# Kernel tuning notes

Hardware: AMD Instinct MI355X
Metric: run time of the kernel (lower is better)

## Reference

```python
import jax, jax.numpy as jnp
import numpy as np

SAMPLE_RATE = 22050
N_FILTER_BANKS = 64
HOP_LENGTH = 512
BATCH = 4
N_FRAMES = 500
N_SAMPLES = N_FRAMES * HOP_LENGTH


def _frame_mean_weights(n_frames, n_samples):
    """Per-frame weights w s.t. mean over time of linear(align_corners=True)
    upsampling of a length-n_frames signal equals w @ signal (exact same math,
    since the interpolation is linear in the frame values)."""
    pos = jnp.linspace(0.0, n_frames - 1.0, n_samples)
    lo = jnp.clip(jnp.floor(pos).astype(jnp.int32), 0, n_frames - 2)
    frac = pos - lo
    w = jnp.zeros(n_frames, dtype=jnp.float32)
    w = w.at[lo].add(1.0 - frac).at[lo + 1].add(frac)
    return w / n_samples


def setup_inputs() -> dict:
    key = jax.random.key(0)
    k1, k2 = jax.random.split(key)
    filter_magnitudes = jax.random.uniform(k1, (BATCH, N_FRAMES, N_FILTER_BANKS), dtype=jnp.float32)
    noise = jax.random.normal(k2, (BATCH, N_SAMPLES), dtype=jnp.float32)
    return {"filter_magnitudes": filter_magnitudes, "noise": noise}


def reference(filter_magnitudes, noise):
    B, n_frames, n_banks = filter_magnitudes.shape
    n_samples = noise.shape[1]

    noise_fft = jnp.fft.rfft(noise, axis=1)                      # (B, n_freq) complex
    freqs = jnp.fft.rfftfreq(n_samples, 1.0 / SAMPLE_RATE)       # (n_freq,)
    filter_freqs = jnp.logspace(np.log10(20.0), np.log10(SAMPLE_RATE / 2.0), n_banks).astype(jnp.float32)

    # mean over time of the linearly-upsampled magnitudes (exact, no big buffer)
    mean_w = _frame_mean_weights(n_frames, n_samples)            # (n_frames,)
    mean_mag = jnp.einsum('bfk,f->bk', filter_magnitudes, mean_w)  # (B, n_banks)

    # vectorized log-distance filterbank weights: (n_freq, n_banks)
    D = jnp.log(freqs + 1e-7)[:, None] - jnp.log(filter_freqs + 1e-7)[None, :]
    W = jnp.exp(-(D ** 2) / 0.5)
    W = W / (W.sum(axis=1, keepdims=True) + 1e-7)

    filter_response = mean_mag @ W.T                              # (B, n_freq)
    filtered_fft = noise_fft * filter_response
    return jnp.fft.irfft(filtered_fft, n=n_samples, axis=1)      # (B, n_samples)
```

## Files before the change

kernel.cpp:

```cpp
#include <hip/hip_runtime.h>
#include <math.h>

#define NS 256000
#define N1 512
#define N2 500
#define PI_F 3.14159265358979323846f

typedef float2 cplx;

__device__ __forceinline__ cplx cadd(cplx a, cplx b){ return make_float2(a.x+b.x, a.y+b.y); }
__device__ __forceinline__ cplx csub(cplx a, cplx b){ return make_float2(a.x-b.x, a.y-b.y); }
__device__ __forceinline__ cplx cmul(cplx a, cplx b){ return make_float2(a.x*b.x-a.y*b.y, a.x*b.y+a.y*b.x); }
__device__ __forceinline__ cplx cmulc(cplx a, cplx b){ return make_float2(a.x*b.x+a.y*b.y, a.y*b.x-a.x*b.y); }
__device__ __forceinline__ cplx crotf(cplx v, float ang){
    float sn = __sinf(ang), cs = __cosf(ang);
    return make_float2(v.x*cs - v.y*sn, v.x*sn + v.y*cs);
}
__device__ __forceinline__ int PX(int e){ return e + (e>>4); }
__device__ __forceinline__ int rev8_3(int k){ return ((k&7)<<6) | (k&0x38) | (k>>6); }

#define U1PAD 545
#define U2PAD 537
#define WFENCE() asm volatile("s_waitcnt lgkmcnt(0)" ::: "memory")

template<bool INV>
__device__ __forceinline__ void dft4(const cplx* a, cplx* b){
    cplx t0=cadd(a[0],a[2]), t1=csub(a[0],a[2]), t2=cadd(a[1],a[3]), t3=csub(a[1],a[3]);
    b[0]=cadd(t0,t2); b[2]=csub(t0,t2);
    if(!INV){ b[1]=make_float2(t1.x+t3.y, t1.y-t3.x); b[3]=make_float2(t1.x-t3.y, t1.y+t3.x); }
    else    { b[1]=make_float2(t1.x-t3.y, t1.y+t3.x); b[3]=make_float2(t1.x+t3.y, t1.y-t3.x); }
}

template<bool INV>
__device__ __forceinline__ void dft8(const cplx* a, cplx* b){
    cplx ev[4]={a[0],a[2],a[4],a[6]}, od[4]={a[1],a[3],a[5],a[7]};
    cplx C[4], D[4];
    dft4<INV>(ev, C); dft4<INV>(od, D);
    const float s = 0.70710678118654752f;
    const float sg = INV ? 1.f : -1.f;
    cplx d1 = cmul(D[1], make_float2( s, sg*s));
    cplx d2 = cmul(D[2], make_float2(0.f, sg ));
    cplx d3 = cmul(D[3], make_float2(-s, sg*s));
    b[0]=cadd(C[0],D[0]); b[4]=csub(C[0],D[0]);
    b[1]=cadd(C[1],d1);   b[5]=csub(C[1],d1);
    b[2]=cadd(C[2],d2);   b[6]=csub(C[2],d2);
    b[3]=cadd(C[3],d3);   b[7]=csub(C[3],d3);
}

template<bool INV>
__device__ __forceinline__ void dft5(const cplx* a, cplx* b){
    const float c1=0.30901699437494742f, s1=0.95105651629515357f;
    const float c2=-0.80901699437494745f, s2=0.58778525229247312f;
    const float sg = INV ? 1.f : -1.f;
    cplx W[5];
    W[0]=make_float2(1.f,0.f);
    W[1]=make_float2(c1, sg*s1); W[2]=make_float2(c2, sg*s2);
    W[3]=make_float2(c2,-sg*s2); W[4]=make_float2(c1,-sg*s1);
#pragma unroll
    for(int u=0;u<5;++u){
        cplx acc = a[0];
        int idx = 0;
#pragma unroll
        for(int r=1;r<5;++r){
            idx += u; if(idx >= 5) idx -= 5;
            acc = cadd(acc, cmul(a[r], W[idx]));
        }
        b[u] = acc;
    }
}

template<int R, int L, int TMUL, bool INV, int NN>
__device__ __forceinline__ void wstage(cplx* Uw, const cplx* tab, int lane){
    constexpr int m = L / R;
    constexpr int nb = NN / R;
    constexpr int NIT = (nb + 63) / 64;
    cplx a[NIT][R];
    cplx wt[NIT][R];
    int  bs[NIT];
#pragma unroll
    for(int it=0; it<NIT; ++it){
        int beta = lane + it*64;
        int blk = beta / m;
        int j = beta - blk*m;
        bs[it] = blk*L + j;
        if(beta < nb){
#pragma unroll
            for(int t=0;t<R;++t) a[it][t] = Uw[PX(bs[it] + m*t)];
#pragma unroll
            for(int t=1;t<R;++t) wt[it][t] = tab[TMUL*j*t];
        }
    }
#pragma unroll
    for(int it=0; it<NIT; ++it){
        int beta = lane + it*64;
        if(beta < nb){
            if(INV){
#pragma unroll
                for(int t=1;t<R;++t) a[it][t] = cmulc(a[it][t], wt[it][t]);
            }
            cplx bb[R];
            if constexpr (R==4) dft4<INV>(a[it], bb);
            else if constexpr (R==5) dft5<INV>(a[it], bb);
            else dft8<INV>(a[it], bb);
            if(!INV){
#pragma unroll
                for(int t=1;t<R;++t) bb[t] = cmul(bb[t], wt[it][t]);
            }
#pragma unroll
            for(int t=0;t<R;++t) Uw[PX(bs[it] + m*t)] = bb[t];
        }
    }
}

template<int NTAB>
__device__ __forceinline__ void build_tab(cplx* tab, int tid){
    const float step = -2.f*PI_F/(float)NTAB;
    for(int i = tid; i < NTAB; i += 128){
        float a = step*(float)i;
        tab[i] = make_float2(__cosf(a), __sinf(a));
    }
}

__device__ __forceinline__ int p2k2(int p){
    int t1 = p/100; int r = p - 100*t1;
    int t2 = r/20;  r -= 20*t2;
    int t3 = r>>2;  int t4 = r & 3;
    return t1 + 5*t2 + 25*t3 + 125*t4;
}
__device__ __forceinline__ int k22p(int k){
    int t1 = k % 5; int k5 = k/5;
    int t2 = k5 % 5; int k25 = k5/5;
    int t3 = k25 % 5; int t4 = k25/5;
    return 100*t1 + 20*t2 + 4*t3 + t4;
}
__device__ __forceinline__ int colord(int q){
    int j = q>>1, w = q&1;
    if(j == 0) return w ? 256 : 0;
    return w ? 512 - j : j;
}
__device__ __forceinline__ int xcd_chunk(int bid, int n){
    int q = n>>3, r = n&7;
    int x = bid&7, idx = bid>>3;
    return (x < r ? x*(q+1) : r*(q+1) + (x-r)*q) + idx;
}

__device__ __forceinline__ void hpair(cplx Z1, cplx Z2, float ha, float hb,
                                      cplx* zk, cplx* znk){
    float xr = 0.5f*(Z1.x + Z2.x), xi = 0.5f*(Z1.y - Z2.y);
    float yr = 0.5f*(Z1.y + Z2.y), yi = -0.5f*(Z1.x - Z2.x);
    *zk  = make_float2(ha*xr - hb*yi, ha*xi + hb*yr);
    *znk = make_float2(ha*xr + hb*yi, hb*yr - ha*xi);
}

__global__ void __launch_bounds__(128) kFused1(const float* __restrict__ fm,
                                               const float* __restrict__ noise,
                                               float* __restrict__ mmL,
                                               cplx* __restrict__ Y){
    __shared__ float Aarr[500];
    __shared__ float wfr[500];
    __shared__ float part[128];
    __shared__ cplx tab[512];
    __shared__ cplx U[2][U1PAD];
    const int bid = blockIdx.x, tid = threadIdx.x;
    if(bid < 4){
        const int b = bid;
        for(int f = tid; f < 500; f += 128){
            long long i0 = ((long long)f*255999LL + 498LL)/499LL;
            long long i1 = ((long long)(f+1)*255999LL + 498LL)/499LL;
            long long cnt = i1 - i0;
            long long sumi = (i0 + i1 - 1)*cnt/2;
            long long num = 499LL*sumi - cnt*(long long)f*255999LL;
            Aarr[f] = (float)((double)num / 255999.0);
        }
        __syncthreads();
        for(int f = tid; f < 500; f += 128){
            long long i0 = ((long long)f*255999LL + 498LL)/499LL;
            long long i1 = ((long long)(f+1)*255999LL + 498LL)/499LL;
            double w;
            if(f < 499) w = (double)(i1 - i0) - (double)Aarr[f] + (f > 0 ? (double)Aarr[f-1] : 0.0);
            else        w = (double)Aarr[498] + 1.0;
            wfr[f] = (float)(w / (double)NS);
        }
        __syncthreads();
        const int k = tid & 63, seg = tid >> 6;
        float acc = 0.f;
        for(int f = seg*250; f < seg*250 + 250; ++f)
            acc += wfr[f] * fm[(b*500 + f)*64 + k];
        part[seg*64 + k] = acc;
        __syncthreads();
        if(tid < 64) mmL[b*64 + tid] = part[tid] + part[64 + tid];
        return;
    }
    if(bid == 4){
        if(tid < 64){
            double a = log10(20.0), b2 = log10(11025.0);
            double e = a + (b2 - a)*(double)tid/63.0;
            float ff = (float)pow(10.0, e);
            mmL[256 + tid] = logf(ff + 1e-7f);
        }
        return;
    }
    const int g = bid - 5;
    const int s = g / 250;
    const int n2base = (g - s*250) * 2;
    const int lane = tid & 63, w = tid >> 6;
    build_tab<512>(tab, tid);
    const float* xa = noise + (size_t)(2*s)*NS + n2base;
    const float* xb = noise + (size_t)(2*s+1)*NS + n2base;
#pragma unroll
    for(int k=0;k<8;++k){
        int i = tid + 128*k;
        int n1 = i >> 1, ws = i & 1;
        U[ws][PX(n1)] = make_float2(xa[n1*500 + ws], xb[n1*500 + ws]);
    }
    __syncthreads();
    cplx* Uw = U[w];
    wstage<8,512, 1,false,512>(Uw, tab, lane); WFENCE();
    wstage<8, 64, 8,false,512>(Uw, tab, lane); WFENCE();
    wstage<8,  8,64,false,512>(Uw, tab, lane); WFENCE();
    const int n2 = n2base + w;
    cplx* yp = Y + ((size_t)s*500 + n2)*512;
    const float tw = -2.f*PI_F/(float)NS;
#pragma unroll
    for(int t=0;t<8;++t){
        int q = lane + 64*t;
        int c = colord(q);
        cplx v = Uw[PX(rev8_3(c))];
        v = crotf(v, tw*(float)(n2*c));
        yp[q] = v;
    }
}

__global__ void __launch_bounds__(128) kFused2(cplx* __restrict__ Y,
                                               const float* __restrict__ mmL){
    __shared__ cplx tab[500];
    __shared__ cplx U[2][U2PAD];
    __shared__ float Hr[4][500];
    __shared__ float mmS[2][64];
    __shared__ float lgf[64];
    const int tid = threadIdx.x, lane = tid & 63, w = tid >> 6;
    const int L = xcd_chunk(blockIdx.x, 512);
    const int s = L >> 8, blk = L & 255;
    build_tab<500>(tab, tid);
    if(tid < 128) mmS[tid>>6][tid&63] = mmL[2*s*64 + tid];
    if(tid < 64)  lgf[tid] = mmL[256 + tid];
    cplx* yb = Y + (size_t)s*500*512 + 2*blk;
    cplx rg[8];
#pragma unroll
    for(int k=0;k<8;++k){
        int i = tid + 128*k;
        rg[k] = (i < 1000) ? yb[(i>>1)*512 + (i&1)] : make_float2(0.f, 0.f);
    }
    __syncthreads();
    const int nrows = (blk == 0) ? 2 : 1;
    const float invN = 1.f/(float)NS;
    for(int idx = tid; idx < nrows*500; idx += 128){
        int r = (idx >= 500) ? 1 : 0;
        int p = idx - 500*r;
        int k1 = (blk == 0) ? (r ? 256 : 0) : blk;
        int k2 = p2k2(p);
        int kf = k1 + 512*k2;
        int kk = min(kf, NS - kf);
        float lf = logf((float)kk*(22050.f/(float)NS) + 1e-7f);
        float wsum = 0.f, a0 = 0.f, a1 = 0.f;
#pragma unroll
        for(int jb=0;jb<64;++jb){
            float d = lf - lgf[jb];
            float e = __expf(-2.f*d*d);
            wsum += e; a0 += e*mmS[0][jb]; a1 += e*mmS[1][jb];
        }
        float inv = invN/(wsum + 1e-7f);
        Hr[2*r  ][p] = a0*inv;
        Hr[2*r+1][p] = a1*inv;
    }
#pragma unroll
    for(int k=0;k<8;++k){
        int i = tid + 128*k;
        if(i < 1000) U[i&1][PX(i>>1)] = rg[k];
    }
    __syncthreads();
    cplx* Uw = U[w];
    wstage<5,500,  1,false,500>(Uw, tab, lane); WFENCE();
    wstage<5,100,  5,false,500>(Uw, tab, lane); WFENCE();
    wstage<5, 20, 25,false,500>(Uw, tab, lane); WFENCE();
    wstage<4,  4,125,false,500>(Uw, tab, lane); WFENCE();
    __syncthreads();
    if(blk == 0){
        if(w == 0){
#pragma unroll
            for(int t=0;t<8;++t){
                int p = lane + 64*t;
                if(p < 500){
                    int k2 = p2k2(p);
                    int pp = k22p((500 - k2) % 500);
                    if(p <= pp){
                        cplx Z1 = U[0][PX(p)], Z2 = U[0][PX(pp)];
                        cplx zk, znk;
                        hpair(Z1, Z2, Hr[0][p], Hr[1][p], &zk, &znk);
                        U[0][PX(p)]  = zk;
                        U[0][PX(pp)] = znk;
                    }
                }
            }
        } else {
#pragma unroll
            for(int t=0;t<4;++t){
                int p = lane + 64*t;
                if(p < 250){
                    cplx Z1 = U[1][PX(p)], Z2 = U[1][PX(499-p)];
                    cplx zk, znk;
                    hpair(Z1, Z2, Hr[2][p], Hr[3][p], &zk, &znk);
                    U[1][PX(p)]     = zk;
                    U[1][PX(499-p)] = znk;
                }
            }
        }
    } else {
#pragma unroll
        for(int t=0;t<4;++t){
            int pl = lane + 64*t;
            if(pl < 250){
                int p = w*250 + pl;
                cplx Z1 = U[0][PX(p)], Z2 = U[1][PX(499-p)];
                cplx zk, znk;
                hpair(Z1, Z2, Hr[0][p], Hr[1][p], &zk, &znk);
                U[0][PX(p)]     = zk;
                U[1][PX(499-p)] = znk;
            }
        }
    }
    __syncthreads();
    wstage<4,  4,125,true,500>(Uw, tab, lane); WFENCE();
    wstage<5, 20, 25,true,500>(Uw, tab, lane); WFENCE();
    wstage<5,100,  5,true,500>(Uw, tab, lane); WFENCE();
    wstage<5,500,  1,true,500>(Uw, tab, lane); WFENCE();
    __syncthreads();
    const float tw = 2.f*PI_F/(float)NS;
#pragma unroll
    for(int k=0;k<8;++k){
        int i = tid + 128*k;
        if(i < 1000){
            int n2 = i >> 1, ws = i & 1;
            int c = colord(2*blk + ws);
            cplx v = U[ws][PX(n2)];
            v = crotf(v, tw*(float)(n2*c));
            yb[n2*512 + ws] = v;
        }
    }
}

__global__ void __launch_bounds__(128) kFused3(const cplx* __restrict__ Y,
                                               float* __restrict__ out){
    __shared__ cplx tab[512];
    __shared__ cplx U[2][U1PAD];
    const int tid = threadIdx.x, lane = tid & 63, w = tid >> 6;
    const int L = xcd_chunk(blockIdx.x, 500);
    const int s = L / 250;
    const int n2base = (L - s*250) * 2;
    build_tab<512>(tab, tid);
    const cplx* yp = Y + ((size_t)s*500 + n2base)*512;
#pragma unroll
    for(int k=0;k<8;++k){
        int i = tid + 128*k;
        int ws = i >> 9, q = i & 511;
        cplx v = yp[(size_t)ws*512 + q];
        U[ws][PX(rev8_3(colord(q)))] = v;
    }
    __syncthreads();
    cplx* Uw = U[w];
    wstage<8,  8,64,true,512>(Uw, tab, lane); WFENCE();
    wstage<8, 64, 8,true,512>(Uw, tab, lane); WFENCE();
    wstage<8,512, 1,true,512>(Uw, tab, lane); WFENCE();
    __syncthreads();
    float* oa = out + (size_t)(2*s)*NS + n2base;
    float* ob = out + (size_t)(2*s+1)*NS + n2base;
#pragma unroll
    for(int k=0;k<8;++k){
        int i = tid + 128*k;
        int n1 = i >> 1, ws = i & 1;
        cplx v = U[ws][PX(n1)];
        oa[n1*500 + ws] = v.x;
        ob[n1*500 + ws] = v.y;
    }
}

extern "C" void kernel_launch(void* const* d_in, const int* in_sizes, int n_in,
                              void* d_out, int out_size, void* d_ws, size_t ws_size,
                              hipStream_t stream) {
    const float* fm = (const float*)d_in[0];
    const float* noise = (const float*)d_in[1];
    float* out = (float*)d_out;

    char* ws = (char*)d_ws;
    cplx*  Y   = (cplx*)ws;
    float* mmL = (float*)(ws + 4200000);

    kFused1<<<505, 128, 0, stream>>>(fm, noise, mmL, Y);
    kFused2<<<512, 128, 0, stream>>>(Y, mmL);
    kFused3<<<500, 128, 0, stream>>>(Y, out);
}
```

Before: 98.65 us.

## Widen FFT kernels to 256 threads and split column FFT stages across two waves

The row-FFT kernels (kFused1, kFused3) now process four columns per 256-thread block instead of two, which halves the number of blocks and shares the twiddle-table build across more work. kFused2 keeps two columns per block but assigns two waves to each column. It splits each radix stage's butterflies between them with a new wstage2 helper, so block-wide barriers are needed between stages. kFused2 also issues its global loads before building the twiddle table, to hide load latency. The aim is higher occupancy and latency hiding, at the cost of more synchronisation and fewer blocks in the first and last kernels.

```diff
diff --git a/kernel.cpp b/kernel.cpp
--- a/kernel.cpp
+++ b/kernel.cpp
@@ -22,6 +22,7 @@
 #define U1PAD 545
 #define U2PAD 537
 #define WFENCE() asm volatile("s_waitcnt lgkmcnt(0)" ::: "memory")
+#define LDS_BARRIER() do{ asm volatile("s_waitcnt lgkmcnt(0)" ::: "memory"); __builtin_amdgcn_s_barrier(); }while(0)
 
 template<bool INV>
 __device__ __forceinline__ void dft4(const cplx* a, cplx* b){
@@ -112,10 +113,44 @@
     }
 }
 
-template<int NTAB>
+template<int R, int L, int TMUL, bool INV>
+__device__ __forceinline__ void wstage2(cplx* Uc, const cplx* tab, int lane, int h){
+    constexpr int m = L / R;
+    constexpr int nb = 500 / R;
+    constexpr int HB = (nb + 1) / 2;
+    const int lim = h ? (nb - HB) : HB;
+    if(lane < lim){
+        int beta = h*HB + lane;
+        int blk = beta / m;
+        int j = beta - blk*m;
+        int base = blk*L + j;
+        cplx a[R];
+#pragma unroll
+        for(int t=0;t<R;++t) a[t] = Uc[PX(base + m*t)];
+        cplx wt[R];
+#pragma unroll
+        for(int t=1;t<R;++t) wt[t] = tab[TMUL*j*t];
+        if(INV){
+#pragma unroll
+            for(int t=1;t<R;++t) a[t] = cmulc(a[t], wt[t]);
+        }
+        cplx bb[R];
+        if constexpr (R==4) dft4<INV>(a,bb);
+        else if constexpr (R==5) dft5<INV>(a,bb);
+        else dft8<INV>(a,bb);
+        if(!INV){
+#pragma unroll
+            for(int t=1;t<R;++t) bb[t] = cmul(bb[t], wt[t]);
+        }
+#pragma unroll
+        for(int t=0;t<R;++t) Uc[PX(base + m*t)] = bb[t];
+    }
+}
+
+template<int NTAB, int NTHR>
 __device__ __forceinline__ void build_tab(cplx* tab, int tid){
     const float step = -2.f*PI_F/(float)NTAB;
-    for(int i = tid; i < NTAB; i += 128){
+    for(int i = tid; i < NTAB; i += NTHR){
         float a = step*(float)i;
         tab[i] = make_float2(__cosf(a), __sinf(a));
     }
@@ -152,19 +187,19 @@
     *znk = make_float2(ha*xr + hb*yi, hb*yr - ha*xi);
 }
 
-__global__ void __launch_bounds__(128) kFused1(const float* __restrict__ fm,
+__global__ void __launch_bounds__(256) kFused1(const float* __restrict__ fm,
                                                const float* __restrict__ noise,
                                                float* __restrict__ mmL,
                                                cplx* __restrict__ Y){
     __shared__ float Aarr[500];
     __shared__ float wfr[500];
-    __shared__ float part[128];
+    __shared__ float part[256];
     __shared__ cplx tab[512];
-    __shared__ cplx U[2][U1PAD];
+    __shared__ cplx U[4][U1PAD];
     const int bid = blockIdx.x, tid = threadIdx.x;
     if(bid < 4){
         const int b = bid;
-        for(int f = tid; f < 500; f += 128){
+        for(int f = tid; f < 500; f += 256){
             long long i0 = ((long long)f*255999LL + 498LL)/499LL;
             long long i1 = ((long long)(f+1)*255999LL + 498LL)/499LL;
             long long cnt = i1 - i0;
@@ -173,7 +208,7 @@
             Aarr[f] = (float)((double)num / 255999.0);
         }
         __syncthreads();
-        for(int f = tid; f < 500; f += 128){
+        for(int f = tid; f < 500; f += 256){
             long long i0 = ((long long)f*255999LL + 498LL)/499LL;
             long long i1 = ((long long)(f+1)*255999LL + 498LL)/499LL;
             double w;
@@ -184,11 +219,11 @@
         __syncthreads();
         const int k = tid & 63, seg = tid >> 6;
         float acc = 0.f;
-        for(int f = seg*250; f < seg*250 + 250; ++f)
+        for(int f = seg*125; f < seg*125 + 125; ++f)
             acc += wfr[f] * fm[(b*500 + f)*64 + k];
         part[seg*64 + k] = acc;
         __syncthreads();
-        if(tid < 64) mmL[b*64 + tid] = part[tid] + part[64 + tid];
+        if(tid < 64) mmL[b*64 + tid] = part[tid] + part[64+tid] + part[128+tid] + part[192+tid];
         return;
     }
     if(bid == 4){
@@ -200,17 +235,17 @@
         }
         return;
     }
-    const int g = bid - 5;
-    const int s = g / 250;
-    const int n2base = (g - s*250) * 2;
+    const int g = xcd_chunk(bid - 5, 250);
+    const int s = g / 125;
+    const int n2base = (g - s*125) * 4;
     const int lane = tid & 63, w = tid >> 6;
-    build_tab<512>(tab, tid);
+    build_tab<512,256>(tab, tid);
     const float* xa = noise + (size_t)(2*s)*NS + n2base;
     const float* xb = noise + (size_t)(2*s+1)*NS + n2base;
 #pragma unroll
     for(int k=0;k<8;++k){
-        int i = tid + 128*k;
-        int n1 = i >> 1, ws = i & 1;
+        int i = tid + 256*k;
+        int n1 = i >> 2, ws = i & 3;
         U[ws][PX(n1)] = make_float2(xa[n1*500 + ws], xb[n1*500 + ws]);
     }
     __syncthreads();
@@ -231,30 +266,30 @@
     }
 }
 
-__global__ void __launch_bounds__(128) kFused2(cplx* __restrict__ Y,
+__global__ void __launch_bounds__(256) kFused2(cplx* __restrict__ Y,
                                                const float* __restrict__ mmL){
     __shared__ cplx tab[500];
     __shared__ cplx U[2][U2PAD];
     __shared__ float Hr[4][500];
     __shared__ float mmS[2][64];
     __shared__ float lgf[64];
-    const int tid = threadIdx.x, lane = tid & 63, w = tid >> 6;
+    const int tid = threadIdx.x, lane = tid & 63, W = tid >> 6;
     const int L = xcd_chunk(blockIdx.x, 512);
     const int s = L >> 8, blk = L & 255;
-    build_tab<500>(tab, tid);
+    cplx* yb = Y + (size_t)s*500*512 + 2*blk;
+    cplx rg[4];
+#pragma unroll
+    for(int k=0;k<4;++k){
+        int i = tid + 256*k;
+        rg[k] = (i < 1000) ? yb[(i>>1)*512 + (i&1)] : make_float2(0.f, 0.f);
+    }
+    build_tab<500,256>(tab, tid);
     if(tid < 128) mmS[tid>>6][tid&63] = mmL[2*s*64 + tid];
     if(tid < 64)  lgf[tid] = mmL[256 + tid];
-    cplx* yb = Y + (size_t)s*500*512 + 2*blk;
-    cplx rg[8];
-#pragma unroll
-    for(int k=0;k<8;++k){
-        int i = tid + 128*k;
-        rg[k] = (i < 1000) ? yb[(i>>1)*512 + (i&1)] : make_float2(0.f, 0.f);
-    }
-    __syncthreads();
+    LDS_BARRIER();
     const int nrows = (blk == 0) ? 2 : 1;
     const float invN = 1.f/(float)NS;
-    for(int idx = tid; idx < nrows*500; idx += 128){
+    for(int idx = tid; idx < nrows*500; idx += 256){
         int r = (idx >= 500) ? 1 : 0;
         int p = idx - 500*r;
         int k1 = (blk == 0) ? (r ? 256 : 0) : blk;
@@ -270,27 +305,28 @@
             wsum += e; a0 += e*mmS[0][jb]; a1 += e*mmS[1][jb];
         }
         float inv = invN/(wsum + 1e-7f);
-        Hr[2*r  ][p] = a0*inv;
-        Hr[2*r+1][p] = a1*inv;
-    }
-#pragma unroll
-    for(int k=0;k<8;++k){
-        int i = tid + 128*k;
+        Hr[0][p] = (r==0) ? a0*inv : Hr[0][p];
+        if(r==0){ Hr[0][p] = a0*inv; Hr[1][p] = a1*inv; }
+        else    { Hr[2][p] = a0*inv; Hr[3][p] = a1*inv; }
+    }
+#pragma unroll
+    for(int k=0;k<4;++k){
+        int i = tid + 256*k;
         if(i < 1000) U[i&1][PX(i>>1)] = rg[k];
     }
     __syncthreads();
-    cplx* Uw = U[w];
-    wstage<5,500,  1,false,500>(Uw, tab, lane); WFENCE();
-    wstage<5,100,  5,false,500>(Uw, tab, lane); WFENCE();
-    wstage<5, 20, 25,false,500>(Uw, tab, lane); WFENCE();
-    wstage<4,  4,125,false,500>(Uw, tab, lane); WFENCE();
-    __syncthreads();
+    const int c = W >> 1, h = W & 1;
+    cplx* Uc = U[c];
+    wstage2<5,500,  1,false>(Uc, tab, lane, h); __syncthreads();
+    wstage2<5,100,  5,false>(Uc, tab, lane, h); __syncthreads();
+    wstage2<5, 20, 25,false>(Uc, tab, lane, h); __syncthreads();
+    wstage2<4,  4,125,false>(Uc, tab, lane, h); __syncthreads();
     if(blk == 0){
-        if(w == 0){
-#pragma unroll
-            for(int t=0;t<8;++t){
-                int p = lane + 64*t;
-                if(p < 500){
+        if(c == 0){
+#pragma unroll
+            for(int t=0;t<4;++t){
+                int p = h*250 + lane + 64*t;
+                if(lane + 64*t < 250){
                     int k2 = p2k2(p);
                     int pp = k22p((500 - k2) % 500);
                     if(p <= pp){
@@ -304,9 +340,10 @@
             }
         } else {
 #pragma unroll
-            for(int t=0;t<4;++t){
-                int p = lane + 64*t;
-                if(p < 250){
+            for(int t=0;t<2;++t){
+                int pl = lane + 64*t;
+                if(pl < 125){
+                    int p = h*125 + pl;
                     cplx Z1 = U[1][PX(p)], Z2 = U[1][PX(499-p)];
                     cplx zk, znk;
                     hpair(Z1, Z2, Hr[2][p], Hr[3][p], &zk, &znk);
@@ -317,10 +354,10 @@
         }
     } else {
 #pragma unroll
-        for(int t=0;t<4;++t){
+        for(int t=0;t<2;++t){
             int pl = lane + 64*t;
-            if(pl < 250){
-                int p = w*250 + pl;
+            if(pl < 125){
+                int p = W*125 + pl;
                 cplx Z1 = U[0][PX(p)], Z2 = U[1][PX(499-p)];
                 cplx zk, znk;
                 hpair(Z1, Z2, Hr[0][p], Hr[1][p], &zk, &znk);
@@ -330,38 +367,37 @@
         }
     }
     __syncthreads();
-    wstage<4,  4,125,true,500>(Uw, tab, lane); WFENCE();
-    wstage<5, 20, 25,true,500>(Uw, tab, lane); WFENCE();
-    wstage<5,100,  5,true,500>(Uw, tab, lane); WFENCE();
-    wstage<5,500,  1,true,500>(Uw, tab, lane); WFENCE();
-    __syncthreads();
+    wstage2<4,  4,125,true>(Uc, tab, lane, h); __syncthreads();
+    wstage2<5, 20, 25,true>(Uc, tab, lane, h); __syncthreads();
+    wstage2<5,100,  5,true>(Uc, tab, lane, h); __syncthreads();
+    wstage2<5,500,  1,true>(Uc, tab, lane, h); __syncthreads();
     const float tw = 2.f*PI_F/(float)NS;
 #pragma unroll
-    for(int k=0;k<8;++k){
-        int i = tid + 128*k;
+    for(int k=0;k<4;++k){
+        int i = tid + 256*k;
         if(i < 1000){
             int n2 = i >> 1, ws = i & 1;
-            int c = colord(2*blk + ws);
+            int cc = colord(2*blk + ws);
             cplx v = U[ws][PX(n2)];
-            v = crotf(v, tw*(float)(n2*c));
+            v = crotf(v, tw*(float)(n2*cc));
             yb[n2*512 + ws] = v;
         }
     }
 }
 
-__global__ void __launch_bounds__(128) kFused3(const cplx* __restrict__ Y,
+__global__ void __launch_bounds__(256) kFused3(const cplx* __restrict__ Y,
                                                float* __restrict__ out){
     __shared__ cplx tab[512];
-    __shared__ cplx U[2][U1PAD];
+    __shared__ cplx U[4][U1PAD];
     const int tid = threadIdx.x, lane = tid & 63, w = tid >> 6;
-    const int L = xcd_chunk(blockIdx.x, 500);
-    const int s = L / 250;
-    const int n2base = (L - s*250) * 2;
-    build_tab<512>(tab, tid);
+    const int g = xcd_chunk(blockIdx.x, 250);
+    const int s = g / 125;
+    const int n2base = (g - s*125) * 4;
+    build_tab<512,256>(tab, tid);
     const cplx* yp = Y + ((size_t)s*500 + n2base)*512;
 #pragma unroll
     for(int k=0;k<8;++k){
-        int i = tid + 128*k;
+        int i = tid + 256*k;
         int ws = i >> 9, q = i & 511;
         cplx v = yp[(size_t)ws*512 + q];
         U[ws][PX(rev8_3(colord(q)))] = v;
@@ -376,8 +412,8 @@
     float* ob = out + (size_t)(2*s+1)*NS + n2base;
 #pragma unroll
     for(int k=0;k<8;++k){
-        int i = tid + 128*k;
-        int n1 = i >> 1, ws = i & 1;
+        int i = tid + 256*k;
+        int n1 = i >> 2, ws = i & 3;
         cplx v = U[ws][PX(n1)];
         oa[n1*500 + ws] = v.x;
         ob[n1*500 + ws] = v.y;
@@ -395,7 +431,7 @@
     cplx*  Y   = (cplx*)ws;
     float* mmL = (float*)(ws + 4200000);
 
-    kFused1<<<505, 128, 0, stream>>>(fm, noise, mmL, Y);
-    kFused2<<<512, 128, 0, stream>>>(Y, mmL);
-    kFused3<<<500, 128, 0, stream>>>(Y, out);
-}
+    kFused1<<<255, 256, 0, stream>>>(fm, noise, mmL, Y);
+    kFused2<<<512, 256, 0, stream>>>(Y, mmL);
+    kFused3<<<250, 256, 0, stream>>>(Y, out);
+}
```

Measured after the change: 93.45 us. 1.06x faster.

## Double per-block FFT work to four columns with 256-thread blocks

Applied to the files above, without the earlier changes.

All three FFT kernels now run 256-thread blocks, each handling four columns or rows instead of two. That halves the grid sizes, gives 4-wide contiguous global accesses, and remaps kFused1 blocks through the XCD chunking. kFused2 loads its global data before building the twiddle table, uses a cheaper LDS barrier, and drops some trailing waitcnt fences. The intent is to cut per-block overhead (twiddle table builds, launch cost) and improve coalescing, at the cost of fewer blocks for the GPU's many CUs and higher LDS use per block.

```diff
diff --git a/kernel.cpp b/kernel.cpp
--- a/kernel.cpp
+++ b/kernel.cpp
@@ -22,6 +22,7 @@
 #define U1PAD 545
 #define U2PAD 537
 #define WFENCE() asm volatile("s_waitcnt lgkmcnt(0)" ::: "memory")
+#define LDS_BARRIER() do{ asm volatile("s_waitcnt lgkmcnt(0)" ::: "memory"); __builtin_amdgcn_s_barrier(); }while(0)
 
 template<bool INV>
 __device__ __forceinline__ void dft4(const cplx* a, cplx* b){
@@ -112,10 +113,10 @@
     }
 }
 
-template<int NTAB>
+template<int NTAB, int NTHR>
 __device__ __forceinline__ void build_tab(cplx* tab, int tid){
     const float step = -2.f*PI_F/(float)NTAB;
-    for(int i = tid; i < NTAB; i += 128){
+    for(int i = tid; i < NTAB; i += NTHR){
         float a = step*(float)i;
         tab[i] = make_float2(__cosf(a), __sinf(a));
     }
@@ -152,19 +153,19 @@
     *znk = make_float2(ha*xr + hb*yi, hb*yr - ha*xi);
 }
 
-__global__ void __launch_bounds__(128) kFused1(const float* __restrict__ fm,
+__global__ void __launch_bounds__(256) kFused1(const float* __restrict__ fm,
                                                const float* __restrict__ noise,
                                                float* __restrict__ mmL,
                                                cplx* __restrict__ Y){
     __shared__ float Aarr[500];
     __shared__ float wfr[500];
-    __shared__ float part[128];
+    __shared__ float part[256];
     __shared__ cplx tab[512];
-    __shared__ cplx U[2][U1PAD];
+    __shared__ cplx U[4][U1PAD];
     const int bid = blockIdx.x, tid = threadIdx.x;
     if(bid < 4){
         const int b = bid;
-        for(int f = tid; f < 500; f += 128){
+        for(int f = tid; f < 500; f += 256){
             long long i0 = ((long long)f*255999LL + 498LL)/499LL;
             long long i1 = ((long long)(f+1)*255999LL + 498LL)/499LL;
             long long cnt = i1 - i0;
@@ -173,7 +174,7 @@
             Aarr[f] = (float)((double)num / 255999.0);
         }
         __syncthreads();
-        for(int f = tid; f < 500; f += 128){
+        for(int f = tid; f < 500; f += 256){
             long long i0 = ((long long)f*255999LL + 498LL)/499LL;
             long long i1 = ((long long)(f+1)*255999LL + 498LL)/499LL;
             double w;
@@ -184,11 +185,11 @@
         __syncthreads();
         const int k = tid & 63, seg = tid >> 6;
         float acc = 0.f;
-        for(int f = seg*250; f < seg*250 + 250; ++f)
+        for(int f = seg*125; f < seg*125 + 125; ++f)
             acc += wfr[f] * fm[(b*500 + f)*64 + k];
         part[seg*64 + k] = acc;
         __syncthreads();
-        if(tid < 64) mmL[b*64 + tid] = part[tid] + part[64 + tid];
+        if(tid < 64) mmL[b*64 + tid] = part[tid] + part[64+tid] + part[128+tid] + part[192+tid];
         return;
     }
     if(bid == 4){
@@ -200,17 +201,17 @@
         }
         return;
     }
-    const int g = bid - 5;
-    const int s = g / 250;
-    const int n2base = (g - s*250) * 2;
+    const int g = xcd_chunk(bid - 5, 250);
+    const int s = g / 125;
+    const int n2base = (g - s*125) * 4;
     const int lane = tid & 63, w = tid >> 6;
-    build_tab<512>(tab, tid);
+    build_tab<512,256>(tab, tid);
     const float* xa = noise + (size_t)(2*s)*NS + n2base;
     const float* xb = noise + (size_t)(2*s+1)*NS + n2base;
 #pragma unroll
     for(int k=0;k<8;++k){
-        int i = tid + 128*k;
-        int n1 = i >> 1, ws = i & 1;
+        int i = tid + 256*k;
+        int n1 = i >> 2, ws = i & 3;
         U[ws][PX(n1)] = make_float2(xa[n1*500 + ws], xb[n1*500 + ws]);
     }
     __syncthreads();
@@ -219,7 +220,7 @@
     wstage<8, 64, 8,false,512>(Uw, tab, lane); WFENCE();
     wstage<8,  8,64,false,512>(Uw, tab, lane); WFENCE();
     const int n2 = n2base + w;
-    cplx* yp = Y + ((size_t)s*500 + n2)*512;
+    cplx* yp = Y + ((size_t)s*500 + n2)*N1;
     const float tw = -2.f*PI_F/(float)NS;
 #pragma unroll
     for(int t=0;t<8;++t){
@@ -231,33 +232,37 @@
     }
 }
 
-__global__ void __launch_bounds__(128) kFused2(cplx* __restrict__ Y,
+__global__ void __launch_bounds__(256) kFused2(cplx* __restrict__ Y,
                                                const float* __restrict__ mmL){
     __shared__ cplx tab[500];
-    __shared__ cplx U[2][U2PAD];
-    __shared__ float Hr[4][500];
+    __shared__ cplx U[4][U2PAD];
+    __shared__ float Hr[2][2][500];
+    __shared__ float HrX[2][500];
     __shared__ float mmS[2][64];
     __shared__ float lgf[64];
     const int tid = threadIdx.x, lane = tid & 63, w = tid >> 6;
-    const int L = xcd_chunk(blockIdx.x, 512);
-    const int s = L >> 8, blk = L & 255;
-    build_tab<500>(tab, tid);
-    if(tid < 128) mmS[tid>>6][tid&63] = mmL[2*s*64 + tid];
+    const int L = xcd_chunk(blockIdx.x, 256);
+    const int su = L >> 7;
+    const int j0 = 2*(L & 127);
+    const int s0 = 2*j0;
+    cplx* Ybase = Y + (size_t)su*500*512 + s0;
+    cplx rg[8];
+#pragma unroll
+    for(int k=0;k<8;++k){
+        int e = tid + 256*k;
+        rg[k] = (e < 2000) ? Ybase[(e>>2)*512 + (e&3)] : make_float2(0.f,0.f);
+    }
+    build_tab<500,256>(tab, tid);
+    if(tid < 128) mmS[tid>>6][tid&63] = mmL[2*su*64 + tid];
     if(tid < 64)  lgf[tid] = mmL[256 + tid];
-    cplx* yb = Y + (size_t)s*500*512 + 2*blk;
-    cplx rg[8];
-#pragma unroll
-    for(int k=0;k<8;++k){
-        int i = tid + 128*k;
-        rg[k] = (i < 1000) ? yb[(i>>1)*512 + (i&1)] : make_float2(0.f, 0.f);
-    }
-    __syncthreads();
-    const int nrows = (blk == 0) ? 2 : 1;
+    LDS_BARRIER();
+    const int special = (j0 == 0);
+    const int nrows = special ? 3 : 2;
     const float invN = 1.f/(float)NS;
-    for(int idx = tid; idx < nrows*500; idx += 128){
-        int r = (idx >= 500) ? 1 : 0;
+    for(int idx = tid; idx < nrows*500; idx += 256){
+        int r = idx / 500;
         int p = idx - 500*r;
-        int k1 = (blk == 0) ? (r ? 256 : 0) : blk;
+        int k1 = (r==0) ? j0 : ((r==1) ? j0+1 : 256);
         int k2 = p2k2(p);
         int kf = k1 + 512*k2;
         int kk = min(kf, NS - kf);
@@ -266,66 +271,73 @@
 #pragma unroll
         for(int jb=0;jb<64;++jb){
             float d = lf - lgf[jb];
-            float e = __expf(-2.f*d*d);
-            wsum += e; a0 += e*mmS[0][jb]; a1 += e*mmS[1][jb];
+            float e2 = __expf(-2.f*d*d);
+            wsum += e2; a0 += e2*mmS[0][jb]; a1 += e2*mmS[1][jb];
         }
         float inv = invN/(wsum + 1e-7f);
-        Hr[2*r  ][p] = a0*inv;
-        Hr[2*r+1][p] = a1*inv;
-    }
-#pragma unroll
-    for(int k=0;k<8;++k){
-        int i = tid + 128*k;
-        if(i < 1000) U[i&1][PX(i>>1)] = rg[k];
+        if(r < 2){ Hr[r][0][p] = a0*inv; Hr[r][1][p] = a1*inv; }
+        else     { HrX[0][p]   = a0*inv; HrX[1][p]   = a1*inv; }
+    }
+#pragma unroll
+    for(int k=0;k<8;++k){
+        int e = tid + 256*k;
+        if(e < 2000) U[e&3][PX(e>>2)] = rg[k];
     }
     __syncthreads();
     cplx* Uw = U[w];
     wstage<5,500,  1,false,500>(Uw, tab, lane); WFENCE();
     wstage<5,100,  5,false,500>(Uw, tab, lane); WFENCE();
     wstage<5, 20, 25,false,500>(Uw, tab, lane); WFENCE();
-    wstage<4,  4,125,false,500>(Uw, tab, lane); WFENCE();
-    __syncthreads();
-    if(blk == 0){
-        if(w == 0){
-#pragma unroll
-            for(int t=0;t<8;++t){
-                int p = lane + 64*t;
-                if(p < 500){
-                    int k2 = p2k2(p);
-                    int pp = k22p((500 - k2) % 500);
-                    if(p <= pp){
-                        cplx Z1 = U[0][PX(p)], Z2 = U[0][PX(pp)];
+    wstage<4,  4,125,false,500>(Uw, tab, lane);
+    __syncthreads();
+    {
+        const int u = w >> 1, cw = w & 1;
+        cplx* UA = U[2*u];
+        cplx* UB = U[2*u + 1];
+        if(special && u == 0){
+            if(cw == 0){
+#pragma unroll 1
+                for(int t=0;t<8;++t){
+                    int p = lane + 64*t;
+                    if(p < 500){
+                        int k2 = p2k2(p);
+                        int pp = k22p((500 - k2) % 500);
+                        if(p <= pp){
+                            cplx Z1 = UA[PX(p)], Z2 = UA[PX(pp)];
+                            cplx zk, znk;
+                            hpair(Z1, Z2, Hr[0][0][p], Hr[0][1][p], &zk, &znk);
+                            UA[PX(p)]  = zk;
+                            UA[PX(pp)] = znk;
+                        }
+                    }
+                }
+            } else {
+#pragma unroll 1
+                for(int t=0;t<4;++t){
+                    int p = lane + 64*t;
+                    if(p < 250){
+                        cplx Z1 = UB[PX(p)], Z2 = UB[PX(499-p)];
                         cplx zk, znk;
-                        hpair(Z1, Z2, Hr[0][p], Hr[1][p], &zk, &znk);
-                        U[0][PX(p)]  = zk;
-                        U[0][PX(pp)] = znk;
+                        hpair(Z1, Z2, HrX[0][p], HrX[1][p], &zk, &znk);
+                        UB[PX(p)]     = zk;
+                        UB[PX(499-p)] = znk;
                     }
                 }
             }
         } else {
-#pragma unroll
+            const float* H0 = Hr[u][0];
+            const float* H1 = Hr[u][1];
+#pragma unroll 1
             for(int t=0;t<4;++t){
-                int p = lane + 64*t;
-                if(p < 250){
-                    cplx Z1 = U[1][PX(p)], Z2 = U[1][PX(499-p)];
+                int pl = lane + 64*t;
+                if(pl < 250){
+                    int p = cw*250 + pl;
+                    cplx Z1 = UA[PX(p)], Z2 = UB[PX(499-p)];
                     cplx zk, znk;
-                    hpair(Z1, Z2, Hr[2][p], Hr[3][p], &zk, &znk);
-                    U[1][PX(p)]     = zk;
-                    U[1][PX(499-p)] = znk;
+                    hpair(Z1, Z2, H0[p], H1[p], &zk, &znk);
+                    UA[PX(p)]     = zk;
+                    UB[PX(499-p)] = znk;
                 }
-            }
-        }
-    } else {
-#pragma unroll
-        for(int t=0;t<4;++t){
-            int pl = lane + 64*t;
-            if(pl < 250){
-                int p = w*250 + pl;
-                cplx Z1 = U[0][PX(p)], Z2 = U[1][PX(499-p)];
-                cplx zk, znk;
-                hpair(Z1, Z2, Hr[0][p], Hr[1][p], &zk, &znk);
-                U[0][PX(p)]     = zk;
-                U[1][PX(499-p)] = znk;
             }
         }
     }
@@ -333,51 +345,51 @@
     wstage<4,  4,125,true,500>(Uw, tab, lane); WFENCE();
     wstage<5, 20, 25,true,500>(Uw, tab, lane); WFENCE();
     wstage<5,100,  5,true,500>(Uw, tab, lane); WFENCE();
-    wstage<5,500,  1,true,500>(Uw, tab, lane); WFENCE();
-    __syncthreads();
-    const float tw = 2.f*PI_F/(float)NS;
-#pragma unroll
-    for(int k=0;k<8;++k){
-        int i = tid + 128*k;
-        if(i < 1000){
-            int n2 = i >> 1, ws = i & 1;
-            int c = colord(2*blk + ws);
-            cplx v = U[ws][PX(n2)];
-            v = crotf(v, tw*(float)(n2*c));
-            yb[n2*512 + ws] = v;
-        }
-    }
-}
-
-__global__ void __launch_bounds__(128) kFused3(const cplx* __restrict__ Y,
+    wstage<5,500,  1,true,500>(Uw, tab, lane);
+    __syncthreads();
+    const float tw2 = 2.f*PI_F/(float)NS;
+#pragma unroll
+    for(int k=0;k<8;++k){
+        int e = tid + 256*k;
+        if(e < 2000){
+            int n2 = e >> 2, sl = e & 3;
+            int cc = colord(s0 + sl);
+            cplx v = U[sl][PX(n2)];
+            v = crotf(v, tw2*(float)(n2*cc));
+            Ybase[n2*512 + sl] = v;
+        }
+    }
+}
+
+__global__ void __launch_bounds__(256) kFused3(const cplx* __restrict__ Y,
                                                float* __restrict__ out){
     __shared__ cplx tab[512];
-    __shared__ cplx U[2][U1PAD];
+    __shared__ cplx U[4][U1PAD];
     const int tid = threadIdx.x, lane = tid & 63, w = tid >> 6;
-    const int L = xcd_chunk(blockIdx.x, 500);
-    const int s = L / 250;
-    const int n2base = (L - s*250) * 2;
-    build_tab<512>(tab, tid);
-    const cplx* yp = Y + ((size_t)s*500 + n2base)*512;
-#pragma unroll
-    for(int k=0;k<8;++k){
-        int i = tid + 128*k;
+    const int g = xcd_chunk(blockIdx.x, 250);
+    const int s = g / 125;
+    const int n2base = (g - s*125) * 4;
+    build_tab<512,256>(tab, tid);
+    const cplx* yp = Y + ((size_t)s*500 + n2base)*N1;
+#pragma unroll
+    for(int k=0;k<8;++k){
+        int i = tid + 256*k;
         int ws = i >> 9, q = i & 511;
-        cplx v = yp[(size_t)ws*512 + q];
+        cplx v = yp[(size_t)ws*N1 + q];
         U[ws][PX(rev8_3(colord(q)))] = v;
     }
     __syncthreads();
     cplx* Uw = U[w];
     wstage<8,  8,64,true,512>(Uw, tab, lane); WFENCE();
     wstage<8, 64, 8,true,512>(Uw, tab, lane); WFENCE();
-    wstage<8,512, 1,true,512>(Uw, tab, lane); WFENCE();
+    wstage<8,512, 1,true,512>(Uw, tab, lane);
     __syncthreads();
     float* oa = out + (size_t)(2*s)*NS + n2base;
     float* ob = out + (size_t)(2*s+1)*NS + n2base;
 #pragma unroll
     for(int k=0;k<8;++k){
-        int i = tid + 128*k;
-        int n1 = i >> 1, ws = i & 1;
+        int i = tid + 256*k;
+        int n1 = i >> 2, ws = i & 3;
         cplx v = U[ws][PX(n1)];
         oa[n1*500 + ws] = v.x;
         ob[n1*500 + ws] = v.y;
@@ -393,9 +405,9 @@
 
     char* ws = (char*)d_ws;
     cplx*  Y   = (cplx*)ws;
-    float* mmL = (float*)(ws + 4200000);
-
-    kFused1<<<505, 128, 0, stream>>>(fm, noise, mmL, Y);
-    kFused2<<<512, 128, 0, stream>>>(Y, mmL);
-    kFused3<<<500, 128, 0, stream>>>(Y, out);
-}
+    float* mmL = (float*)(ws + 4194304);
+
+    kFused1<<<255, 256, 0, stream>>>(fm, noise, mmL, Y);
+    kFused2<<<256, 256, 0, stream>>>(Y, mmL);
+    kFused3<<<250, 256, 0, stream>>>(Y, out);
+}
```

Result: faster. 90.59 us (-8.2%).
